# Kernel tuning notes

Hardware: AMD Instinct MI355X
Metric: run time of the kernel (lower is better)

Reference implementation:

```python
import jax, jax.numpy as jnp
import numpy as np
from jax import lax

K = 7          # kernel size
G = 12         # groups
EPS = 1e-5


def bn(x, gamma, beta, axes):
    # training-mode batch norm (torch default train() mode uses batch stats)
    mean = jnp.mean(x, axis=axes, keepdims=True)
    var = jnp.var(x, axis=axes, keepdims=True)
    shape = [1] * x.ndim
    shape[1 if x.ndim == 4 else -1] = -1
    g = gamma.reshape(shape)
    b = beta.reshape(shape)
    return g * (x - mean) * lax.rsqrt(var + EPS) + b


def setup_inputs() -> dict:
    key = jax.random.key(0)
    ks = jax.random.split(key, 12)
    B, C, H, Wd = 16, 192, 32, 32
    Cr = C // 4                      # reduce_mapping out channels = out_channels // reduce_ratio = 48
    flat = C * H * Wd                # 196608
    inp = {
        "x": jax.random.normal(ks[0], (B, C, H, Wd), jnp.float32),
        "Wr": jax.random.normal(ks[1], (Cr, C), jnp.float32) * 0.05,          # reduce_mapping 1x1 conv
        "gamma_s": jnp.ones((Cr,), jnp.float32),
        "beta_s": jnp.zeros((Cr,), jnp.float32),
        "Ws": jax.random.normal(ks[2], (K * K * G, Cr), jnp.float32) * 0.05,  # span_mapping 1x1 conv
        "W1": jax.random.normal(ks[3], (512, flat), jnp.float32) * 0.002,
        "b1": jnp.zeros((512,), jnp.float32),
        "g1": jnp.ones((512,), jnp.float32),
        "beta1": jnp.zeros((512,), jnp.float32),
        "W2": jax.random.normal(ks[4], (128, 512), jnp.float32) * 0.04,
        "b2": jnp.zeros((128,), jnp.float32),
        "g2": jnp.ones((128,), jnp.float32),
        "beta2": jnp.zeros((128,), jnp.float32),
        "W3": jax.random.normal(ks[5], (17, 128), jnp.float32) * 0.09,
        "b3": jnp.zeros((17,), jnp.float32),
    }
    return inp


def reference(x, Wr, gamma_s, beta_s, Ws, W1, b1, g1, beta1, W2, b2, g2, beta2, W3, b3):
    B, C, H, Wd = x.shape
    Cg = C // G
    # unfold (im2col) with kernel 7, pad 3, stride 1, dil 1 -> [B, C*K*K, H, W]
    # channel ordering (c, kh, kw) matches torch.nn.Unfold
    patches = lax.conv_general_dilated_patches(x, (K, K), (1, 1), [(K // 2, K // 2)] * 2)
    unf = patches.reshape(B, G, Cg, K * K, H, Wd)
    # kernel generation path: 1x1 reduce conv -> BN+ReLU -> 1x1 span conv
    red = jnp.einsum('bchw,oc->bohw', x, Wr)
    red = jax.nn.relu(bn(red, gamma_s, beta_s, (0, 2, 3)))
    ker = jnp.einsum('bchw,oc->bohw', red, Ws).reshape(B, G, K * K, H, Wd)
    # involution: per-pixel kernel multiply + sum over K*K
    out = jnp.einsum('bgkhw,bgckhw->bgchw', ker, unf).reshape(B, C, H, Wd)
    # classifier head
    flat = out.reshape(B, -1)
    h = jax.nn.relu(bn(flat @ W1.T + b1, g1, beta1, (0,)))
    h = jax.nn.relu(bn(h @ W2.T + b2, g2, beta2, (0,)))
    return h @ W3.T + b3
```

## Files before the change

kernel.cpp:

```cpp
#include <hip/hip_runtime.h>

#define EPS 1e-5f

typedef float v4f __attribute__((ext_vector_type(4)));

__global__ __launch_bounds__(256) void k_reduce_conv(
    const float* __restrict__ x, const float* __restrict__ Wr,
    float* __restrict__ red, float* __restrict__ spart)
{
  int ob = blockIdx.x >> 6;
  int pb = blockIdx.x & 63;
  int o0 = ob * 6;
  int pix = (pb << 8) + threadIdx.x;
  int b = pix >> 10;
  int hw = pix & 1023;
  const float* xp = x + ((size_t)b * 192) * 1024 + hw;
  float acc[6] = {0.f, 0.f, 0.f, 0.f, 0.f, 0.f};
  for (int c = 0; c < 192; ++c) {
    float xv = xp[(size_t)c * 1024];
#pragma unroll
    for (int j = 0; j < 6; ++j)
      acc[j] = fmaf(xv, Wr[(o0 + j) * 192 + c], acc[j]);
  }
#pragma unroll
  for (int j = 0; j < 6; ++j)
    red[(size_t)(o0 + j) * 16384 + pix] = acc[j];

  int t = threadIdx.x, lane = t & 63, wid = t >> 6;
  float sv[6], qv[6];
#pragma unroll
  for (int j = 0; j < 6; ++j) { sv[j] = acc[j]; qv[j] = acc[j] * acc[j]; }
#pragma unroll
  for (int off = 32; off > 0; off >>= 1)
#pragma unroll
    for (int j = 0; j < 6; ++j) {
      sv[j] += __shfl_down(sv[j], off);
      qv[j] += __shfl_down(qv[j], off);
    }
  __shared__ float ps[4][12];
  if (lane == 0)
#pragma unroll
    for (int j = 0; j < 6; ++j) { ps[wid][j] = sv[j]; ps[wid][6 + j] = qv[j]; }
  __syncthreads();
  if (t < 12) {
    float v = ps[0][t] + ps[1][t] + ps[2][t] + ps[3][t];
    int j = t % 6, s = t / 6;
    spart[(size_t)(s * 48 + o0 + j) * 64 + pb] = v;
  }
}

__global__ __launch_bounds__(256) void k_invol(
    const float* __restrict__ x, const float* __restrict__ red,
    const float* __restrict__ spart, const float* __restrict__ gamma_s,
    const float* __restrict__ beta_s, const float* __restrict__ Ws,
    float* __restrict__ flat)
{
  __shared__ __align__(16) float xt[196 * 20];
  __shared__ __align__(16) float redn[64 * 52];
  __shared__ __align__(16) float kt[49 * 64];
  __shared__ float sstats[96];

  int bx = blockIdx.x;
  int tile = bx & 15;
  int g = (bx >> 4) % 12;
  int b = bx / 192;
  int th = (tile >> 2) * 8, tw = (tile & 3) * 8;
  int t = threadIdx.x;

  if (t < 96) {
    const v4f* p = (const v4f*)(spart + (size_t)t * 64);
    v4f s4 = p[0];
#pragma unroll
    for (int i = 1; i < 16; ++i) s4 += p[i];
    sstats[t] = s4.x + s4.y + s4.z + s4.w;
  }

  for (int idx = t; idx < 16 * 196; idx += 256) {
    int c = idx / 196, s = idx - c * 196;
    int r = s / 14, q = s - r * 14;
    int sh = th + r - 3, sw = tw + q - 3;
    float v = 0.f;
    if (sh >= 0 && sh < 32 && sw >= 0 && sw < 32)
      v = x[(((size_t)b * 192 + g * 16 + c) << 10) + (sh << 5) + sw];
    xt[s * 20 + c] = v;
  }
  __syncthreads();

  for (int idx = t; idx < 64 * 48; idx += 256) {
    int p = idx & 63, o = idx >> 6;
    int py = p >> 3, px = p & 7;
    float mean = sstats[o] * (1.f / 16384.f);
    float var = fmaf(-mean, mean, sstats[48 + o] * (1.f / 16384.f));
    float sc = gamma_s[o] * rsqrtf(var + EPS);
    float sh_ = fmaf(-mean, sc, beta_s[o]);
    float v = red[(size_t)o * 16384 + (b << 10) + ((th + py) << 5) + (tw + px)];
    redn[p * 52 + o] = fmaxf(fmaf(v, sc, sh_), 0.f);
  }
  __syncthreads();

  {
    int p = t & 63;
    int kg = __builtin_amdgcn_readfirstlane(t >> 6);
    int k0 = kg * 13;
    float acc[13];
#pragma unroll
    for (int j = 0; j < 13; ++j) acc[j] = 0.f;
    const float* wsp = Ws + (size_t)(g * 49 + k0) * 48;
    for (int o4 = 0; o4 < 48; o4 += 4) {
      v4f rv = *(const v4f*)&redn[p * 52 + o4];
#pragma unroll
      for (int j = 0; j < 13; ++j)
        if (k0 + j < 49) {
          acc[j] = fmaf(rv.x, wsp[j * 48 + o4 + 0], acc[j]);
          acc[j] = fmaf(rv.y, wsp[j * 48 + o4 + 1], acc[j]);
          acc[j] = fmaf(rv.z, wsp[j * 48 + o4 + 2], acc[j]);
          acc[j] = fmaf(rv.w, wsp[j * 48 + o4 + 3], acc[j]);
        }
    }
#pragma unroll
    for (int j = 0; j < 13; ++j)
      if (k0 + j < 49) kt[(k0 + j) * 64 + p] = acc[j];
  }
  __syncthreads();

  {
    int p = t & 63, cq = t >> 6;
    int c0 = cq * 4;
    int py = p >> 3, px = p & 7;
    float a0 = 0.f, a1 = 0.f, a2 = 0.f, a3 = 0.f;
#pragma unroll
    for (int k = 0; k < 49; ++k) {
      int dh = k / 7, dw = k - dh * 7;
      float kv = kt[k * 64 + p];
      const v4f xv = *(const v4f*)&xt[((py + dh) * 14 + px + dw) * 20 + c0];
      a0 = fmaf(kv, xv.x, a0);
      a1 = fmaf(kv, xv.y, a1);
      a2 = fmaf(kv, xv.z, a2);
      a3 = fmaf(kv, xv.w, a3);
    }
    size_t base = (((size_t)b * 192 + g * 16 + c0) << 10) + ((th + py) << 5) + (tw + px);
    flat[base] = a0;
    flat[base + 1024] = a1;
    flat[base + 2048] = a2;
    flat[base + 3072] = a3;
  }
}

__global__ __launch_bounds__(256) void k_gemm1(
    const float* __restrict__ flat, const float* __restrict__ W1,
    float* __restrict__ h1part)
{
  int kc = blockIdx.x;
  int n0 = blockIdx.y * 8;
  int t = threadIdx.x;

  const v4f* W1v = (const v4f*)W1;
  const v4f* flatv = (const v4f*)flat;

  float acc[8][16];
#pragma unroll
  for (int n = 0; n < 8; ++n)
#pragma unroll
    for (int b = 0; b < 16; ++b) acc[n][b] = 0.f;

  int kv = kc * 6144 + t;
  v4f wv[8], wvn[8];
#pragma unroll
  for (int n = 0; n < 8; ++n)
    wv[n] = __builtin_nontemporal_load(&W1v[(size_t)(n0 + n) * 49152 + kv]);

  for (int it = 0; it < 24; ++it) {
    if (it < 23) {
#pragma unroll
      for (int n = 0; n < 8; ++n)
        wvn[n] = __builtin_nontemporal_load(&W1v[(size_t)(n0 + n) * 49152 + kv + 256]);
    }
    v4f fv = flatv[kv];
#pragma unroll
    for (int b = 0; b < 16; ++b) {
      v4f fn;
      if (b < 15) fn = flatv[(size_t)(b + 1) * 49152 + kv];
#pragma unroll
      for (int n = 0; n < 8; ++n) {
        acc[n][b] = fmaf(wv[n].x, fv.x, acc[n][b]);
        acc[n][b] = fmaf(wv[n].y, fv.y, acc[n][b]);
        acc[n][b] = fmaf(wv[n].z, fv.z, acc[n][b]);
        acc[n][b] = fmaf(wv[n].w, fv.w, acc[n][b]);
      }
      fv = fn;
    }
    if (it < 23) {
#pragma unroll
      for (int n = 0; n < 8; ++n) wv[n] = wvn[n];
    }
    kv += 256;
  }

  __shared__ float rbuf[256 * 33];
#pragma unroll
  for (int pass = 0; pass < 4; ++pass) {
    __syncthreads();
#pragma unroll
    for (int nn = 0; nn < 2; ++nn)
#pragma unroll
      for (int b = 0; b < 16; ++b)
        rbuf[t * 33 + nn * 16 + b] = acc[pass * 2 + nn][b];
    __syncthreads();
    int v = t >> 3, i = t & 7;
    float s = 0.f;
#pragma unroll
    for (int j = 0; j < 32; ++j)
      s += rbuf[(i + (j << 3)) * 33 + v];
    s += __shfl_down(s, 4, 8);
    s += __shfl_down(s, 2, 8);
    s += __shfl_down(s, 1, 8);
    if (i == 0) {
      int nn = v >> 4, b = v & 15;
      h1part[(size_t)kc * 8192 + b * 512 + n0 + pass * 2 + nn] = s;
    }
  }
}

__global__ __launch_bounds__(256) void k_gemm2(
    const float* __restrict__ h1part, const float* __restrict__ g1,
    const float* __restrict__ beta1, const float* __restrict__ W2,
    float* __restrict__ h2pre)
{
  __shared__ __align__(16) float h1s[2][512];
  int t = threadIdx.x;
  int b0 = blockIdx.x * 2;

#pragma unroll
  for (int rep = 0; rep < 2; ++rep) {
    int n = rep * 256 + t;
    float v[16];
#pragma unroll
    for (int b = 0; b < 16; ++b) v[b] = 0.f;
    for (int y = 0; y < 8; ++y)
#pragma unroll
      for (int b = 0; b < 16; ++b)
        v[b] += h1part[(size_t)y * 8192 + b * 512 + n];
    float s = 0.f;
#pragma unroll
    for (int b = 0; b < 16; ++b) s += v[b];
    float mean = s * (1.f / 16.f);
    float q = 0.f;
#pragma unroll
    for (int b = 0; b < 16; ++b) { float d = v[b] - mean; q = fmaf(d, d, q); }
    float inv = rsqrtf(q * (1.f / 16.f) + EPS);
    float sc = g1[n] * inv, sh = beta1[n];
    h1s[0][n] = fmaxf(fmaf(v[b0] - mean, sc, sh), 0.f);
    h1s[1][n] = fmaxf(fmaf(v[b0 + 1] - mean, sc, sh), 0.f);
  }
  __syncthreads();

  int m = t & 127, bsel = t >> 7;
  const v4f* W2v = (const v4f*)W2;
  v4f sa = {0.f, 0.f, 0.f, 0.f};
  for (int nv = 0; nv < 128; ++nv) {
    v4f wv = W2v[(size_t)m * 128 + nv];
    v4f hv = *(const v4f*)&h1s[bsel][nv * 4];
    sa.x = fmaf(hv.x, wv.x, sa.x);
    sa.y = fmaf(hv.y, wv.y, sa.y);
    sa.z = fmaf(hv.z, wv.z, sa.z);
    sa.w = fmaf(hv.w, wv.w, sa.w);
  }
  h2pre[(b0 + bsel) * 128 + m] = (sa.x + sa.y) + (sa.z + sa.w);
}

__global__ __launch_bounds__(320) void k_tail(
    const float* __restrict__ h2pre, const float* __restrict__ g2,
    const float* __restrict__ beta2, const float* __restrict__ W3,
    const float* __restrict__ b3, float* __restrict__ out)
{
  __shared__ float h2[16 * 128];
  int t = threadIdx.x;
  if (t < 128) {
    float v[16];
    float s = 0.f;
#pragma unroll
    for (int b = 0; b < 16; ++b) { v[b] = h2pre[b * 128 + t]; s += v[b]; }
    float mean = s * (1.f / 16.f);
    float q = 0.f;
#pragma unroll
    for (int b = 0; b < 16; ++b) { float d = v[b] - mean; q = fmaf(d, d, q); }
    float inv = rsqrtf(q * (1.f / 16.f) + EPS);
    float sc = g2[t] * inv, sh = beta2[t];
#pragma unroll
    for (int b = 0; b < 16; ++b)
      h2[b * 128 + t] = fmaxf(fmaf(v[b] - mean, sc, sh), 0.f);
  }
  __syncthreads();
  if (t < 272) {
    int b = t / 17, j = t - b * 17;
    float s = b3[j];
    const float* hp = h2 + b * 128;
    const float* wp = W3 + j * 128;
#pragma unroll 4
    for (int m = 0; m < 128; ++m) s = fmaf(hp[m], wp[m], s);
    out[t] = s;
  }
}

extern "C" void kernel_launch(void* const* d_in, const int* in_sizes, int n_in,
                              void* d_out, int out_size, void* d_ws, size_t ws_size,
                              hipStream_t stream)
{
  const float* x       = (const float*)d_in[0];
  const float* Wr      = (const float*)d_in[1];
  const float* gamma_s = (const float*)d_in[2];
  const float* beta_s  = (const float*)d_in[3];
  const float* Ws      = (const float*)d_in[4];
  const float* W1      = (const float*)d_in[5];
  const float* g1      = (const float*)d_in[7];
  const float* beta1   = (const float*)d_in[8];
  const float* W2      = (const float*)d_in[9];
  const float* g2      = (const float*)d_in[11];
  const float* beta2   = (const float*)d_in[12];
  const float* W3      = (const float*)d_in[13];
  const float* b3      = (const float*)d_in[14];

  float* ws = (float*)d_ws;
  float* red    = ws;
  float* flat   = red + 786432;
  float* spart  = flat + 3145728;
  float* h1part = spart + 6144;
  float* h2pre  = h1part + 65536;

  k_reduce_conv<<<512, 256, 0, stream>>>(x, Wr, red, spart);
  k_invol<<<3072, 256, 0, stream>>>(x, red, spart, gamma_s, beta_s, Ws, flat);
  k_gemm1<<<dim3(8, 64), 256, 0, stream>>>(flat, W1, h1part);
  k_gemm2<<<8, 256, 0, stream>>>(h1part, g1, beta1, W2, h2pre);
  k_tail<<<1, 320, 0, stream>>>(h2pre, g2, beta2, W3, b3, (float*)d_out);
}
```

Measured before the change: 276.1 us.

## Halve gemm1 output tile per block and ping-pong unrolled weight prefetch

The W1 GEMV-like kernel now handles 4 output rows per block instead of 8, doubling the grid to 1024 blocks. This cuts accumulator registers so more waves can be resident. The K loop is manually unrolled into two phases that alternate between weight buffers, removing the register copies, and all 16 batch rows of flat are loaded up front. The trade-off is that flat activations are read twice as many times in total, and more partial sums are written.

```diff
diff --git a/kernel.cpp b/kernel.cpp
--- a/kernel.cpp
+++ b/kernel.cpp
@@ -151,54 +151,58 @@
     float* __restrict__ h1part)
 {
   int kc = blockIdx.x;
-  int n0 = blockIdx.y * 8;
+  int n0 = blockIdx.y * 4;
   int t = threadIdx.x;
 
   const v4f* W1v = (const v4f*)W1;
   const v4f* flatv = (const v4f*)flat;
 
-  float acc[8][16];
-#pragma unroll
-  for (int n = 0; n < 8; ++n)
+  float acc[4][16];
+#pragma unroll
+  for (int n = 0; n < 4; ++n)
 #pragma unroll
     for (int b = 0; b < 16; ++b) acc[n][b] = 0.f;
 
   int kv = kc * 6144 + t;
-  v4f wv[8], wvn[8];
-#pragma unroll
-  for (int n = 0; n < 8; ++n)
-    wv[n] = __builtin_nontemporal_load(&W1v[(size_t)(n0 + n) * 49152 + kv]);
-
-  for (int it = 0; it < 24; ++it) {
-    if (it < 23) {
-#pragma unroll
-      for (int n = 0; n < 8; ++n)
-        wvn[n] = __builtin_nontemporal_load(&W1v[(size_t)(n0 + n) * 49152 + kv + 256]);
-    }
-    v4f fv = flatv[kv];
-#pragma unroll
-    for (int b = 0; b < 16; ++b) {
-      v4f fn;
-      if (b < 15) fn = flatv[(size_t)(b + 1) * 49152 + kv];
-#pragma unroll
-      for (int n = 0; n < 8; ++n) {
-        acc[n][b] = fmaf(wv[n].x, fv.x, acc[n][b]);
-        acc[n][b] = fmaf(wv[n].y, fv.y, acc[n][b]);
-        acc[n][b] = fmaf(wv[n].z, fv.z, acc[n][b]);
-        acc[n][b] = fmaf(wv[n].w, fv.w, acc[n][b]);
-      }
-      fv = fn;
-    }
-    if (it < 23) {
-#pragma unroll
-      for (int n = 0; n < 8; ++n) wv[n] = wvn[n];
-    }
-    kv += 256;
-  }
+
+  v4f w[4], wn[4], f[16];
+#pragma unroll
+  for (int n = 0; n < 4; ++n)
+    w[n] = __builtin_nontemporal_load(&W1v[(size_t)(n0 + n) * 49152 + kv]);
+
+#define GEMM1_PHASE(CUR, NXT, PRE)                                         \
+  {                                                                        \
+    _Pragma("unroll")                                                      \
+    for (int b = 0; b < 16; ++b)                                           \
+      f[b] = flatv[(size_t)b * 49152 + kv];                                \
+    if (PRE) {                                                             \
+      _Pragma("unroll")                                                    \
+      for (int n = 0; n < 4; ++n)                                          \
+        NXT[n] = __builtin_nontemporal_load(                               \
+            &W1v[(size_t)(n0 + n) * 49152 + kv + 256]);                    \
+    }                                                                      \
+    _Pragma("unroll")                                                      \
+    for (int b = 0; b < 16; ++b)                                           \
+      _Pragma("unroll")                                                    \
+      for (int n = 0; n < 4; ++n) {                                        \
+        acc[n][b] = fmaf(CUR[n].x, f[b].x, acc[n][b]);                     \
+        acc[n][b] = fmaf(CUR[n].y, f[b].y, acc[n][b]);                     \
+        acc[n][b] = fmaf(CUR[n].z, f[b].z, acc[n][b]);                     \
+        acc[n][b] = fmaf(CUR[n].w, f[b].w, acc[n][b]);                     \
+      }                                                                    \
+    kv += 256;                                                             \
+  }
+
+#pragma unroll 1
+  for (int it = 0; it < 12; ++it) {
+    GEMM1_PHASE(w, wn, true)
+    GEMM1_PHASE(wn, w, (it < 11))
+  }
+#undef GEMM1_PHASE
 
   __shared__ float rbuf[256 * 33];
 #pragma unroll
-  for (int pass = 0; pass < 4; ++pass) {
+  for (int pass = 0; pass < 2; ++pass) {
     __syncthreads();
 #pragma unroll
     for (int nn = 0; nn < 2; ++nn)
@@ -329,7 +333,7 @@
 
   k_reduce_conv<<<512, 256, 0, stream>>>(x, Wr, red, spart);
   k_invol<<<3072, 256, 0, stream>>>(x, red, spart, gamma_s, beta_s, Ws, flat);
-  k_gemm1<<<dim3(8, 64), 256, 0, stream>>>(flat, W1, h1part);
+  k_gemm1<<<dim3(8, 128), 256, 0, stream>>>(flat, W1, h1part);
   k_gemm2<<<8, 256, 0, stream>>>(h1part, g1, beta1, W2, h2pre);
   k_tail<<<1, 320, 0, stream>>>(h2pre, g2, beta2, W3, b3, (float*)d_out);
 }
```

Result: slower. 301.8 us (+9.3%).
